# Kernel tuning notes

Measured on AMD Instinct MI355X. Metric: run time of the kernel, lower is better.

Reference implementation:

```python
import jax, jax.numpy as jnp
import numpy as np

B, Z, H, TC, TD, DOUT = 128, 512, 512, 16, 16, 176
DIN_DEC = DOUT + H  # 688: concat(prev_note, conductor_embedding)


def setup_inputs() -> dict:
    key = jax.random.key(0)
    ks = jax.random.split(key, 24)

    def glorot(k, shape):
        lim = np.sqrt(6.0 / (shape[0] + shape[1]))
        return jax.random.uniform(k, shape, jnp.float32, -lim, lim)

    return {
        'z_ssm_embedding': jax.random.normal(ks[0], (B, Z), jnp.float32),
        'pianoroll': jax.random.uniform(ks[1], (B, TC * TD, DOUT), jnp.float32),
        'ssm': jax.random.uniform(ks[2], (B, TC * TD, TC * TD), jnp.float32),
        # z -> conductor initial states (h1,c1,h2,c2), tanh dense
        'Wz': glorot(ks[3], (Z, 4 * H)), 'bz': jnp.zeros((4 * H,), jnp.float32),
        # conductor 2-layer LSTM (input 512)
        'cond_W1': glorot(ks[4], (H, 4 * H)), 'cond_U1': glorot(ks[5], (H, 4 * H)), 'cond_b1': jnp.zeros((4 * H,), jnp.float32),
        'cond_W2': glorot(ks[6], (H, 4 * H)), 'cond_U2': glorot(ks[7], (H, 4 * H)), 'cond_b2': jnp.zeros((4 * H,), jnp.float32),
        # conductor embedding -> decoder initial states, tanh dense
        'Wcd': glorot(ks[8], (H, 4 * H)), 'bcd': jnp.zeros((4 * H,), jnp.float32),
        # core decoder 2-layer LSTM (input 688)
        'dec_W1': glorot(ks[9], (DIN_DEC, 4 * H)), 'dec_U1': glorot(ks[10], (H, 4 * H)), 'dec_b1': jnp.zeros((4 * H,), jnp.float32),
        'dec_W2': glorot(ks[11], (H, 4 * H)), 'dec_U2': glorot(ks[12], (H, 4 * H)), 'dec_b2': jnp.zeros((4 * H,), jnp.float32),
        # output projection (softmax)
        'Wp': glorot(ks[13], (H, DOUT)), 'bp': jnp.zeros((DOUT,), jnp.float32),
    }


def _lstm_step(x, h, c, W, U, b):
    g = x @ W + h @ U + b  # (B, 4H), keras gate order i,f,g,o
    i, f, gg, o = jnp.split(g, 4, axis=-1)
    c = jax.nn.sigmoid(f) * c + jax.nn.sigmoid(i) * jnp.tanh(gg)
    h = jax.nn.sigmoid(o) * jnp.tanh(c)
    return h, c


def reference(z_ssm_embedding, pianoroll, ssm,
              Wz, bz,
              cond_W1, cond_U1, cond_b1, cond_W2, cond_U2, cond_b2,
              Wcd, bcd,
              dec_W1, dec_U1, dec_b1, dec_W2, dec_U2, dec_b2,
              Wp, bp):
    b = z_ssm_embedding.shape[0]
    # conductor initial states from latent (tanh dense, split per layer h/c)
    s = jnp.tanh(z_ssm_embedding @ Wz + bz)
    ch1, cc1, ch2, cc2 = jnp.split(s, 4, axis=-1)
    # In the source, conductor_input and conductor_states are never updated
    # across the outer loop, so the conductor embedding is identical for all
    # 16 segments: compute the single step once.
    x0 = jnp.zeros((b, H), jnp.float32)
    h1, _ = _lstm_step(x0, ch1, cc1, cond_W1, cond_U1, cond_b1)
    cond_emb, _ = _lstm_step(h1, ch2, cc2, cond_W2, cond_U2, cond_b2)  # (B, H)
    # decoder initial states from conductor embedding (same for all segments)
    sd = jnp.tanh(cond_emb @ Wcd + bcd)
    dh1, dc1, dh2, dc2 = jnp.split(sd, 4, axis=-1)

    def seg(note_prev, _):
        def step(carry, _):
            h1, c1, h2, c2, note = carry
            x = jnp.concatenate([note, cond_emb], axis=-1)  # (B, 688)
            h1, c1 = _lstm_step(x, h1, c1, dec_W1, dec_U1, dec_b1)
            h2, c2 = _lstm_step(h1, h2, c2, dec_W2, dec_U2, dec_b2)
            note = jax.nn.softmax(h2 @ Wp + bp, axis=-1)  # output projection
            return (h1, c1, h2, c2, note), note
        (_, _, _, _, note_last), notes = jax.lax.scan(
            step, (dh1, dc1, dh2, dc2, note_prev), None, length=TD)
        return note_last, notes  # notes: (TD, B, DOUT)

    note0 = jnp.zeros((b, DOUT), jnp.float32)
    _, all_notes = jax.lax.scan(seg, note0, None, length=TC)  # (TC, TD, B, DOUT)
    return all_notes.reshape(TC * TD, b, DOUT).transpose(1, 0, 2)  # (B, 256, 176)
```

## Files before the change

### kernel.cpp

```cpp
#include <hip/hip_runtime.h>
#include <hip/hip_bf16.h>
#include <math.h>

#define Bn    128
#define NGn   2048
#define TTn   256
#define DOn   176
#define NBLK  256
#define NTHR  1024
#define HPAR  65536
#define ACC_PAR 24576

typedef unsigned int uint;
using f32x4 = __attribute__((ext_vector_type(4))) float;
using s16x8 = __attribute__((ext_vector_type(8))) short;
union FR { uint u[4]; s16x8 s; };

struct KA {
  const float *z,*Wz,*bz,*cU1,*cb1,*cW2,*cU2,*cb2,*Wcd,*bcd;
  const float *dW1,*dU1,*db1,*dW2,*dU2,*db2,*Wp,*bp;
  float *zT,*sT,*ggate,*h1cT,*ceT,*sdT,*beffP,*db1P,*db2P,*WEp,*out;
  uint *WAh,*WAl,*WBh,*WBl,*h1pk,*h2pk,*dh1pk,*dh2pk;
  int  *accI;
};

__device__ unsigned g_cnt_l1[16 * 32];
__device__ unsigned g_cnt;
__device__ unsigned g_gen;
__device__ unsigned pod_ctr[8 * 64];

__device__ __forceinline__ float sigm(float x) { return 1.0f / (1.0f + __expf(-x)); }

__device__ __forceinline__ float aloadF(const float* p) {
  return __hip_atomic_load(p, __ATOMIC_RELAXED, __HIP_MEMORY_SCOPE_AGENT);
}
__device__ __forceinline__ void astoreF(float* p, float v) {
  __hip_atomic_store(p, v, __ATOMIC_RELAXED, __HIP_MEMORY_SCOPE_AGENT);
}
__device__ __forceinline__ uint aloadU(const uint* p) {
  return __hip_atomic_load(p, __ATOMIC_RELAXED, __HIP_MEMORY_SCOPE_AGENT);
}
__device__ __forceinline__ void astoreU(uint* p, uint v) {
  __hip_atomic_store(p, v, __ATOMIC_RELAXED, __HIP_MEMORY_SCOPE_AGENT);
}
__device__ __forceinline__ int aloadI(const int* p) {
  return __hip_atomic_load(p, __ATOMIC_RELAXED, __HIP_MEMORY_SCOPE_AGENT);
}

__device__ __forceinline__ void split2(float v, unsigned short& h, unsigned short& l) {
  __hip_bfloat16 bh = __float2bfloat16(v);
  float hf = __bfloat162float(bh);
  __hip_bfloat16 bl = __float2bfloat16(v - hf);
  h = *(unsigned short*)&bh; l = *(unsigned short*)&bl;
}
__device__ __forceinline__ uint packsplit(float v) {
  unsigned short h, l; split2(v, h, l);
  return (uint)h | ((uint)l << 16);
}

__device__ __forceinline__ void gbar() {
  __syncthreads();
  if (threadIdx.x == 0) {
    asm volatile("s_waitcnt vmcnt(0)" ::: "memory");
    unsigned g0 = __hip_atomic_load(&g_gen, __ATOMIC_RELAXED, __HIP_MEMORY_SCOPE_AGENT);
    unsigned p1 = __hip_atomic_fetch_add(&g_cnt_l1[(blockIdx.x >> 4) * 32], 1u,
                                         __ATOMIC_RELAXED, __HIP_MEMORY_SCOPE_AGENT);
    if (p1 == 15u) {
      unsigned p2 = __hip_atomic_fetch_add(&g_cnt, 1u, __ATOMIC_RELAXED, __HIP_MEMORY_SCOPE_AGENT);
      if (p2 == 15u) {
        #pragma unroll
        for (int i = 0; i < 16; i++)
          __hip_atomic_store(&g_cnt_l1[i * 32], 0u, __ATOMIC_RELAXED, __HIP_MEMORY_SCOPE_AGENT);
        __hip_atomic_store(&g_cnt, 0u, __ATOMIC_RELAXED, __HIP_MEMORY_SCOPE_AGENT);
        asm volatile("s_waitcnt vmcnt(0)" ::: "memory");
        __hip_atomic_fetch_add(&g_gen, 1u, __ATOMIC_RELAXED, __HIP_MEMORY_SCOPE_AGENT);
      }
    }
    while (__hip_atomic_load(&g_gen, __ATOMIC_RELAXED, __HIP_MEMORY_SCOPE_AGENT) == g0)
      __builtin_amdgcn_s_sleep(1);
  }
  __syncthreads();
}

__device__ __forceinline__ void pbar2(int pod, unsigned& tgt) {
  __syncthreads();
  if (threadIdx.x == 0) {
    asm volatile("s_waitcnt vmcnt(0)" ::: "memory");
    unsigned* ctr = &pod_ctr[pod * 64];
    __hip_atomic_fetch_add(ctr, 1u, __ATOMIC_RELAXED, __HIP_MEMORY_SCOPE_AGENT);
    while ((int)(__hip_atomic_load(ctr, __ATOMIC_RELAXED, __HIP_MEMORY_SCOPE_AGENT) - tgt) < 0) { }
  }
  __syncthreads();
  tgt += 32;
}

__device__ __forceinline__ void stageN(float* __restrict__ xs, const float* __restrict__ X,
                                       int nrows, int b0, int tid) {
  for (int i = tid; i < nrows * 16; i += NTHR)
    xs[i] = aloadF(X + (size_t)(i >> 4) * Bn + b0 + (i & 15));
}

template<int KC>
__device__ __forceinline__ void gemm16(const float* __restrict__ Wb, int colbase,
                                       int kq, int cg, int bg,
                                       const float* __restrict__ xsrc, float acc[16]) {
  const float* wp = Wb + (size_t)(kq * KC) * NGn + colbase + cg * 4;
  const float* xp = xsrc + (kq * KC) * 16 + bg * 4;
  #pragma unroll 2
  for (int kk = 0; kk < KC; kk++) {
    const float4 w4 = *(const float4*)(wp);
    const float4 x4 = *(const float4*)(xp);
    acc[0]  = fmaf(w4.x, x4.x, acc[0]);  acc[1]  = fmaf(w4.x, x4.y, acc[1]);
    acc[2]  = fmaf(w4.x, x4.z, acc[2]);  acc[3]  = fmaf(w4.x, x4.w, acc[3]);
    acc[4]  = fmaf(w4.y, x4.x, acc[4]);  acc[5]  = fmaf(w4.y, x4.y, acc[5]);
    acc[6]  = fmaf(w4.y, x4.z, acc[6]);  acc[7]  = fmaf(w4.y, x4.w, acc[7]);
    acc[8]  = fmaf(w4.z, x4.x, acc[8]);  acc[9]  = fmaf(w4.z, x4.y, acc[9]);
    acc[10] = fmaf(w4.z, x4.z, acc[10]); acc[11] = fmaf(w4.z, x4.w, acc[11]);
    acc[12] = fmaf(w4.w, x4.x, acc[12]); acc[13] = fmaf(w4.w, x4.y, acc[13]);
    acc[14] = fmaf(w4.w, x4.z, acc[14]); acc[15] = fmaf(w4.w, x4.w, acc[15]);
    wp += NGn; xp += 16;
  }
}

__device__ __forceinline__ void pstore(float* __restrict__ part, int kq, int cg, int bg,
                                       const float acc[16]) {
  #pragma unroll
  for (int c = 0; c < 4; c++) {
    float* p = part + (size_t)(kq * 64 + cg * 4 + c) * 17 + bg * 4;
    *(float4*)p = make_float4(acc[c*4], acc[c*4+1], acc[c*4+2], acc[c*4+3]);
  }
}

template<int MODE>
__device__ __forceinline__ void epi_plain(const float* bias, float* out,
                                          int colbase, int b0, int tid,
                                          const float* __restrict__ part) {
  int cl = tid >> 4, bl = tid & 15;
  float s = 0.0f;
  #pragma unroll
  for (int w = 0; w < 8; w++) s += part[(w * 64 + cl) * 17 + bl];
  if (bias) s += bias[colbase + cl];
  if (MODE == 0) s = tanhf(s);
  astoreF(out + (size_t)(colbase + cl) * Bn + b0 + bl, s);
}

__device__ __forceinline__ void cond_nl(const float* gb, const float* cbias,
                                        const float* cin, float* hout, int bid, int tid) {
  int i = bid * NTHR + tid;
  if (i < 512 * Bn) {
    int hid = i >> 7, b = i & 127;
    float gi = aloadF(gb + (size_t)hid * Bn + b)            + cbias[hid];
    float gf = aloadF(gb + (size_t)(512 + hid) * Bn + b)    + cbias[512 + hid];
    float gg = aloadF(gb + (size_t)(1024 + hid) * Bn + b)   + cbias[1024 + hid];
    float go = aloadF(gb + (size_t)(1536 + hid) * Bn + b)   + cbias[1536 + hid];
    float cprev = aloadF(cin + (size_t)hid * Bn + b);
    float c = sigm(gf) * cprev + sigm(gi) * tanhf(gg);
    astoreF(hout + (size_t)hid * Bn + b, sigm(go) * tanhf(c));
  }
}

__device__ __forceinline__ void ldxK(const uint* __restrict__ base, FR& xh, FR& xl) {
  uint w[8];
  #pragma unroll
  for (int e = 0; e < 8; e++) w[e] = aloadU(base + e * 128);
  xh.u[0] = (w[0] & 0xffffu) | (w[1] << 16); xl.u[0] = (w[0] >> 16) | (w[1] & 0xffff0000u);
  xh.u[1] = (w[2] & 0xffffu) | (w[3] << 16); xl.u[1] = (w[2] >> 16) | (w[3] & 0xffff0000u);
  xh.u[2] = (w[4] & 0xffffu) | (w[5] << 16); xl.u[2] = (w[4] >> 16) | (w[5] & 0xffff0000u);
  xh.u[3] = (w[6] & 0xffffu) | (w[7] << 16); xl.u[3] = (w[6] >> 16) | (w[7] & 0xffff0000u);
}
__device__ __forceinline__ void ldxL17(const uint* __restrict__ p, FR& xh, FR& xl) {
  uint w[8];
  #pragma unroll
  for (int e = 0; e < 8; e++) w[e] = p[e * 17];
  xh.u[0] = (w[0] & 0xffffu) | (w[1] << 16); xl.u[0] = (w[0] >> 16) | (w[1] & 0xffff0000u);
  xh.u[1] = (w[2] & 0xffffu) | (w[3] << 16); xl.u[1] = (w[2] >> 16) | (w[3] & 0xffff0000u);
  xh.u[2] = (w[4] & 0xffffu) | (w[5] << 16); xl.u[2] = (w[4] >> 16) | (w[5] & 0xffff0000u);
  xh.u[3] = (w[6] & 0xffffu) | (w[7] << 16); xl.u[3] = (w[6] >> 16) | (w[7] & 0xffff0000u);
}

struct MC {
  const uint *WAh,*WAl,*WBh,*WBl,*dh1pk,*dh2pk;
  uint *h1pk,*h2pk;
  const float *beffP,*db2P,*Wp,*bp;
  int *accI;
  float *out;
  uint *NTu;
  float *plog,*gbuf,*cst,*h2s;
  int j, b0;
};

#define MFMA3(ACC, XH, XL, WH, WL)                                            \
  ACC = __builtin_amdgcn_mfma_f32_16x16x32_bf16(XH.s, WH.s, ACC, 0, 0, 0);    \
  ACC = __builtin_amdgcn_mfma_f32_16x16x32_bf16(XL.s, WH.s, ACC, 0, 0, 0);    \
  ACC = __builtin_amdgcn_mfma_f32_16x16x32_bf16(XH.s, WL.s, ACC, 0, 0, 0);

__device__ __forceinline__ void phaseA(const MC& c, int t, bool doLSTM) {
  const int tid = threadIdx.x, wid = tid >> 6, lane = tid & 63;
  const int m = lane & 15, kh = lane >> 4;
  const int par = t & 1; const bool rst = (t & 15) == 0;
  if (t > 0) {
    const int wv = wid;
    const int* ai = c.accI + ((par ^ 1) * ACC_PAR) + wv * 192;
    float lg[3], pv[3];
    #pragma unroll
    for (int rep = 0; rep < 3; rep++) {
      int o = lane + rep * 64;
      lg[rep] = (o < DOn) ? (float)aloadI(ai + o) * (1.0f / 1048576.0f) + c.bp[o] : -1e30f;
    }
    float mx = fmaxf(fmaxf(lg[0], lg[1]), lg[2]);
    #pragma unroll
    for (int d = 1; d < 64; d <<= 1) mx = fmaxf(mx, __shfl_xor(mx, d));
    float sum = 0.f;
    #pragma unroll
    for (int rep = 0; rep < 3; rep++) {
      int o = lane + rep * 64;
      pv[rep] = (o < DOn) ? __expf(lg[rep] - mx) : 0.f;
      sum += pv[rep];
    }
    #pragma unroll
    for (int d = 1; d < 64; d <<= 1) sum += __shfl_xor(sum, d);
    const float inv = 1.0f / sum;
    #pragma unroll
    for (int rep = 0; rep < 3; rep++) {
      int o = lane + rep * 64;
      float p = pv[rep] * inv;
      c.NTu[o * 17 + wv] = (o < DOn) ? packsplit(p) : 0u;
      if (c.j < 16 && wv == c.j && o < DOn)
        c.out[((size_t)(c.b0 + c.j) * TTn + (t - 1)) * DOn + o] = p;
    }
  }
  __syncthreads();
  if (!doLSTM) return;
  const int nt = wid & 3, ksq = wid >> 2;
  const int s0 = (ksq == 0) ? 0 : (ksq == 1) ? 6 : (ksq == 2) ? 12 : 17;
  const int s1 = (ksq == 0) ? 6 : (ksq == 1) ? 12 : (ksq == 2) ? 17 : 22;
  const uint* hb = (rst ? c.dh1pk : (c.h1pk + (par ^ 1) * HPAR)) + kh * 8 * 128 + c.b0 + m;
  f32x4 acc = {0.f,0.f,0.f,0.f};
  for (int ks = s0; ks < s1; ks++) {
    FR xh, xl;
    if (ks < 6) ldxL17(c.NTu + (ks * 32 + kh * 8) * 17 + m, xh, xl);
    else        ldxK(hb + (ks * 32 - 192) * 128, xh, xl);
    FR wh, wl;
    *(uint4*)wh.u = *(const uint4*)(c.WAh + (size_t)c.j * 22528 + (ks * 4 + nt) * 256 + lane * 4);
    *(uint4*)wl.u = *(const uint4*)(c.WAl + (size_t)c.j * 22528 + (ks * 4 + nt) * 256 + lane * 4);
    MFMA3(acc, xh, xl, wh, wl)
  }
  #pragma unroll
  for (int r = 0; r < 4; r++) c.plog[((ksq * 4 + nt) * 4 + r) * 64 + lane] = acc[r];
  __syncthreads();
  {
    int cl = tid >> 4, bl = tid & 15;
    float s = 0.f;
    #pragma unroll
    for (int k2 = 0; k2 < 4; k2++)
      s += c.plog[((k2 * 4 + (cl >> 4)) * 4 + (bl & 3)) * 64 + (bl >> 2) * 16 + (cl & 15)];
    c.gbuf[cl * 16 + bl] = s + c.beffP[(size_t)(c.j * 64 + cl) * Bn + c.b0 + bl];
  }
  __syncthreads();
  if (tid < 256) {
    int h = tid >> 4, bl = tid & 15;
    float gi = c.gbuf[(h*4+0)*16+bl], gf = c.gbuf[(h*4+1)*16+bl];
    float gg = c.gbuf[(h*4+2)*16+bl], go = c.gbuf[(h*4+3)*16+bl];
    float cp = rst ? c.cst[512 + tid] : c.cst[tid];
    float cc = sigm(gf) * cp + sigm(gi) * tanhf(gg);
    c.cst[tid] = cc;
    astoreU(c.h1pk + par * HPAR + (size_t)(c.j * 16 + h) * 128 + c.b0 + bl,
            packsplit(sigm(go) * tanhf(cc)));
  }
}

__device__ __forceinline__ void phaseB(const MC& c, int t) {
  const int tid = threadIdx.x, wid = tid >> 6, lane = tid & 63;
  const int m = lane & 15, kh = lane >> 4;
  const int nt = wid & 3, ksq = wid >> 2;
  const int par = t & 1; const bool rst = (t & 15) == 0;
  const uint* s1b = c.h1pk + par * HPAR + kh * 8 * 128 + c.b0 + m;
  const uint* s2b = (rst ? c.dh2pk : (c.h2pk + (par ^ 1) * HPAR)) + kh * 8 * 128 + c.b0 + m;
  f32x4 acc = {0.f,0.f,0.f,0.f};
  #pragma unroll
  for (int kk = 0; kk < 8; kk++) {
    const int ks = ksq * 8 + kk;
    FR xh, xl;
    if (ksq < 2) ldxK(s1b + ks * 32 * 128, xh, xl);
    else         ldxK(s2b + (ks - 16) * 32 * 128, xh, xl);
    FR wh, wl;
    *(uint4*)wh.u = *(const uint4*)(c.WBh + (size_t)c.j * 32768 + (ks * 4 + nt) * 256 + lane * 4);
    *(uint4*)wl.u = *(const uint4*)(c.WBl + (size_t)c.j * 32768 + (ks * 4 + nt) * 256 + lane * 4);
    MFMA3(acc, xh, xl, wh, wl)
  }
  #pragma unroll
  for (int r = 0; r < 4; r++) c.plog[((ksq * 4 + nt) * 4 + r) * 64 + lane] = acc[r];
  __syncthreads();
  {
    int cl = tid >> 4, bl = tid & 15;
    float s = 0.f;
    #pragma unroll
    for (int k2 = 0; k2 < 4; k2++)
      s += c.plog[((k2 * 4 + (cl >> 4)) * 4 + (bl & 3)) * 64 + (bl >> 2) * 16 + (cl & 15)];
    c.gbuf[cl * 16 + bl] = s + c.db2P[c.j * 64 + cl];
  }
  __syncthreads();
  if (tid < 256) {
    int h = tid >> 4, bl = tid & 15;
    float gi = c.gbuf[(h*4+0)*16+bl], gf = c.gbuf[(h*4+1)*16+bl];
    float gg = c.gbuf[(h*4+2)*16+bl], go = c.gbuf[(h*4+3)*16+bl];
    float cp = rst ? c.cst[768 + tid] : c.cst[256 + tid];
    float cc = sigm(gf) * cp + sigm(gi) * tanhf(gg);
    c.cst[256 + tid] = cc;
    float h2v = sigm(go) * tanhf(cc);
    c.h2s[h * 16 + bl] = h2v;
    astoreU(c.h2pk + par * HPAR + (size_t)(c.j * 16 + h) * 128 + c.b0 + bl, packsplit(h2v));
  }
  __syncthreads();
  const int o = tid & 255, q = tid >> 8;
  if (o < DOn) {
    float wv[16];
    #pragma unroll
    for (int h = 0; h < 16; h++) wv[h] = c.Wp[(size_t)(c.j * 16 + h) * DOn + o];
    #pragma unroll
    for (int rep = 0; rep < 4; rep++) {
      const int bl = q * 4 + rep;
      float s = 0.f;
      #pragma unroll
      for (int h = 0; h < 16; h++) s = fmaf(c.h2s[h * 16 + bl], wv[h], s);
      __hip_atomic_fetch_add(c.accI + par * ACC_PAR + bl * 192 + o,
                             __float2int_rn(s * 1048576.0f),
                             __ATOMIC_RELAXED, __HIP_MEMORY_SCOPE_AGENT);
    }
  }
  if (tid < 96)
    astoreU((uint*)(c.accI + (par ^ 1) * ACC_PAR + c.j * 96 + tid), 0u);
}

__global__ void __launch_bounds__(NTHR, 1)
hd_kernel(KA A) {
  __shared__ float buf[25088];
  float* xs = buf;
  float* part = buf + 16384;
  const int bid = blockIdx.x, tid = threadIdx.x;
  const int lane = tid & 63;
  const int kqP = tid >> 6, cgP = lane & 15, bgP = lane >> 4;
  const int rP = bid & 31, btP = bid >> 5;
  const int htP = (rP & 7) * 4 + (rP >> 3);
  const int colbaseP = htP * 64, b0P = btP * 16;
  const int pod = bid >> 5;

  unsigned tgt = __hip_atomic_load(&pod_ctr[pod * 64], __ATOMIC_RELAXED,
                                   __HIP_MEMORY_SCOPE_AGENT) + 32;

  {
    const int i0 = bid * NTHR + tid;
    if (i0 < 512 * Bn) { int zb = i0 >> 9, zk = i0 & 511; astoreF(A.zT + (size_t)zk * Bn + zb, A.z[i0]); }
    if (i0 < NGn) {
      int hid = i0 >> 2, g = i0 & 3, sc = g * 512 + hid;
      astoreF(A.db1P + i0, A.db1[sc]);
      astoreF(A.db2P + i0, A.db2[sc]);
    }
    if (i0 < 2 * ACC_PAR) astoreU((uint*)(A.accI + i0), 0u);
    for (int i = i0; i < 512 * NGn; i += NBLK * NTHR) {
      int k = i >> 11, pc = i & 2047;
      int hid = pc >> 2, g = pc & 3;
      astoreF(A.WEp + i, A.dW1[(size_t)(176 + k) * NGn + g * 512 + hid]);
    }
    for (int i = i0; i < 720896; i += NBLK * NTHR) {
      int col = i & 2047, kp = i >> 11, k = kp * 2;
      float w0, w1;
      if (k < 176)      { w0 = A.dW1[(size_t)k * NGn + col];       w1 = A.dW1[(size_t)(k + 1) * NGn + col]; }
      else if (k < 192) { w0 = 0.f; w1 = 0.f; }
      else              { w0 = A.dU1[(size_t)(k - 192) * NGn + col]; w1 = A.dU1[(size_t)(k - 191) * NGn + col]; }
      unsigned short h0, l0, h1, l1; split2(w0, h0, l0); split2(w1, h1, l1);
      int g = col >> 9, hid = col & 511;
      int jj = hid >> 4, cl = (hid & 15) * 4 + g;
      int nt = cl >> 4, n = cl & 15;
      int ks = k >> 5, kr = k & 31, lh = kr >> 3, q = (kr >> 1) & 3;
      int idx = ((jj * 22 + ks) * 4 + nt) * 256 + (lh * 16 + n) * 4 + q;
      astoreU(A.WAh + idx, (uint)h0 | ((uint)h1 << 16));
      astoreU(A.WAl + idx, (uint)l0 | ((uint)l1 << 16));
    }
  }
  gbar();
  {
    stageN(xs, A.zT, 512, b0P, tid); __syncthreads();
    if (tid < 512) {
      float acc[16] = {0,0,0,0,0,0,0,0,0,0,0,0,0,0,0,0};
      gemm16<64>(A.Wz, colbaseP, kqP, cgP, bgP, xs, acc);
      pstore(part, kqP, cgP, bgP, acc);
    }
    __syncthreads();
    epi_plain<0>(A.bz, A.sT, colbaseP, b0P, tid, part);
  }
  gbar();
  {
    stageN(xs, A.sT, 512, b0P, tid); __syncthreads();
    if (tid < 512) {
      float acc[16] = {0,0,0,0,0,0,0,0,0,0,0,0,0,0,0,0};
      gemm16<64>(A.cU1, colbaseP, kqP, cgP, bgP, xs, acc);
      pstore(part, kqP, cgP, bgP, acc);
    }
    __syncthreads();
    epi_plain<1>(nullptr, A.ggate, colbaseP, b0P, tid, part);
  }
  gbar();
  cond_nl(A.ggate, A.cb1, A.sT + (size_t)512 * Bn, A.h1cT, bid, tid);
  gbar();
  {
    stageN(xs, A.h1cT, 512, b0P, tid);
    stageN(xs + 8192, A.sT + (size_t)1024 * Bn, 512, b0P, tid);
    __syncthreads();
    if (tid < 512) {
      float acc[16] = {0,0,0,0,0,0,0,0,0,0,0,0,0,0,0,0};
      gemm16<64>(A.cW2, colbaseP, kqP, cgP, bgP, xs, acc);
      gemm16<64>(A.cU2, colbaseP, kqP, cgP, bgP, xs + 8192, acc);
      pstore(part, kqP, cgP, bgP, acc);
    }
    __syncthreads();
    epi_plain<1>(nullptr, A.ggate, colbaseP, b0P, tid, part);
  }
  gbar();
  cond_nl(A.ggate, A.cb2, A.sT + (size_t)1536 * Bn, A.ceT, bid, tid);
  gbar();
  {
    stageN(xs, A.ceT, 512, b0P, tid); __syncthreads();
    if (tid < 512) {
      float acc[16] = {0,0,0,0,0,0,0,0,0,0,0,0,0,0,0,0};
      gemm16<64>(A.Wcd, colbaseP, kqP, cgP, bgP, xs, acc);
      pstore(part, kqP, cgP, bgP, acc);
    }
    __syncthreads();
    epi_plain<0>(A.bcd, A.sdT, colbaseP, b0P, tid, part);
    __syncthreads();
    if (tid < 512) {
      float acc[16] = {0,0,0,0,0,0,0,0,0,0,0,0,0,0,0,0};
      gemm16<64>(A.WEp, colbaseP, kqP, cgP, bgP, xs, acc);
      pstore(part, kqP, cgP, bgP, acc);
    }
    __syncthreads();
    epi_plain<1>(A.db1P, A.beffP, colbaseP, b0P, tid, part);
  }
  gbar();
  {
    const int i0 = bid * NTHR + tid;
    for (int i = i0; i < 1048576; i += NBLK * NTHR) {
      int col = i & 2047, kp = i >> 11, k = kp * 2;
      float w0, w1;
      if (k < 512) { w0 = A.dW2[(size_t)k * NGn + col];         w1 = A.dW2[(size_t)(k + 1) * NGn + col]; }
      else         { w0 = A.dU2[(size_t)(k - 512) * NGn + col]; w1 = A.dU2[(size_t)(k - 511) * NGn + col]; }
      unsigned short h0, l0, h1, l1; split2(w0, h0, l0); split2(w1, h1, l1);
      int g = col >> 9, hid = col & 511;
      int jj = hid >> 4, cl = (hid & 15) * 4 + g;
      int nt = cl >> 4, n = cl & 15;
      int ks = k >> 5, kr = k & 31, lh = kr >> 3, q = (kr >> 1) & 3;
      int idx = ((jj * 32 + ks) * 4 + nt) * 256 + (lh * 16 + n) * 4 + q;
      astoreU(A.WBh + idx, (uint)h0 | ((uint)h1 << 16));
      astoreU(A.WBl + idx, (uint)l0 | ((uint)l1 << 16));
    }
    if (i0 < 512 * Bn) {
      int hid = i0 >> 7, b = i0 & 127;
      astoreU(A.dh1pk + hid * 128 + b, packsplit(aloadF(A.sdT + (size_t)hid * Bn + b)));
      astoreU(A.dh2pk + hid * 128 + b, packsplit(aloadF(A.sdT + (size_t)(1024 + hid) * Bn + b)));
    }
  }
  gbar();

  MC c;
  c.WAh = A.WAh; c.WAl = A.WAl; c.WBh = A.WBh; c.WBl = A.WBl;
  c.dh1pk = A.dh1pk; c.dh2pk = A.dh2pk;
  c.h1pk = A.h1pk; c.h2pk = A.h2pk;
  c.beffP = A.beffP; c.db2P = A.db2P; c.Wp = A.Wp; c.bp = A.bp; c.out = A.out;
  c.accI = A.accI + pod * 3072;
  c.NTu = (uint*)buf;
  c.plog = buf + 3264;
  c.gbuf = buf + 7360;
  c.cst  = buf + 8384;
  c.h2s  = buf + 9408;
  c.j = bid & 31;
  c.b0 = pod * 16;
  if (tid < 256) {
    int h = tid >> 4, bl = tid & 15;
    c.cst[512 + tid] = aloadF(A.sdT + (size_t)(512 + c.j * 16 + h) * Bn + c.b0 + bl);
    c.cst[768 + tid] = aloadF(A.sdT + (size_t)(1536 + c.j * 16 + h) * Bn + c.b0 + bl);
  }
  for (int i = tid; i < 3264; i += NTHR) c.NTu[i] = 0u;
  __syncthreads();

  for (int t = 0; t < TTn; t++) {
    phaseA(c, t, true);
    pbar2(pod, tgt);
    phaseB(c, t);
    pbar2(pod, tgt);
  }
  phaseA(c, TTn, false);
}

extern "C" void kernel_launch(void* const* d_in, const int* in_sizes, int n_in,
                              void* d_out, int out_size, void* d_ws, size_t ws_size,
                              hipStream_t stream) {
  (void)in_sizes; (void)n_in; (void)out_size; (void)ws_size;
  KA a;
  a.z   = (const float*)d_in[0];
  a.Wz  = (const float*)d_in[3];  a.bz  = (const float*)d_in[4];
  a.cU1 = (const float*)d_in[6];  a.cb1 = (const float*)d_in[7];
  a.cW2 = (const float*)d_in[8];  a.cU2 = (const float*)d_in[9];  a.cb2 = (const float*)d_in[10];
  a.Wcd = (const float*)d_in[11]; a.bcd = (const float*)d_in[12];
  a.dW1 = (const float*)d_in[13]; a.dU1 = (const float*)d_in[14]; a.db1 = (const float*)d_in[15];
  a.dW2 = (const float*)d_in[16]; a.dU2 = (const float*)d_in[17]; a.db2 = (const float*)d_in[18];
  a.Wp  = (const float*)d_in[19]; a.bp  = (const float*)d_in[20];

  float* ws = (float*)d_ws;
  size_t off = 0;
  a.zT    = ws + off; off += (size_t)512  * Bn;
  a.sT    = ws + off; off += (size_t)NGn  * Bn;
  a.ggate = ws + off; off += (size_t)NGn  * Bn;
  a.h1cT  = ws + off; off += (size_t)512  * Bn;
  a.ceT   = ws + off; off += (size_t)512  * Bn;
  a.sdT   = ws + off; off += (size_t)NGn  * Bn;
  a.beffP = ws + off; off += (size_t)NGn  * Bn;
  a.db1P  = ws + off; off += (size_t)NGn;
  a.db2P  = ws + off; off += (size_t)NGn;
  a.WEp   = ws + off; off += (size_t)512 * NGn;
  a.WBh   = (uint*)a.WEp;
  a.WBl   = (uint*)(ws + off); off += (size_t)1048576;
  a.WAh   = (uint*)(ws + off); off += (size_t)720896;
  a.WAl   = (uint*)(ws + off); off += (size_t)720896;
  a.h1pk  = (uint*)(ws + off); off += (size_t)2 * HPAR;
  a.h2pk  = (uint*)(ws + off); off += (size_t)2 * HPAR;
  a.dh1pk = (uint*)(ws + off); off += (size_t)HPAR;
  a.dh2pk = (uint*)(ws + off); off += (size_t)HPAR;
  a.accI  = (int*)(ws + off);  off += (size_t)2 * ACC_PAR;
  a.out   = (float*)d_out;

  hd_kernel<<<dim3(NBLK), dim3(NTHR), 0, stream>>>(a);
}
```

Measured before the change: 7.773 ms.

## Split prep and recurrent decoder into two kernels with 64-block pods

```diff
diff --git a/kernel.cpp b/kernel.cpp
--- a/kernel.cpp
+++ b/kernel.cpp
@@ -7,11 +7,13 @@
 #define TTn   256
 #define DOn   176
 #define NBLK  256
+#define NBLKM 64
 #define NTHR  1024
 #define HPAR  65536
 #define ACC_PAR 24576
 
 typedef unsigned int uint;
+typedef unsigned long long u64;
 using f32x4 = __attribute__((ext_vector_type(4))) float;
 using s16x8 = __attribute__((ext_vector_type(8))) short;
 union FR { uint u[4]; s16x8 s; };
@@ -27,7 +29,7 @@
 __device__ unsigned g_cnt_l1[16 * 32];
 __device__ unsigned g_cnt;
 __device__ unsigned g_gen;
-__device__ unsigned pod_ctr[8 * 64];
+__device__ unsigned pod_slot[8 * 8 * 32];
 
 __device__ __forceinline__ float sigm(float x) { return 1.0f / (1.0f + __expf(-x)); }
 
@@ -44,6 +46,9 @@
   __hip_atomic_store(p, v, __ATOMIC_RELAXED, __HIP_MEMORY_SCOPE_AGENT);
 }
 __device__ __forceinline__ int aloadI(const int* p) {
+  return __hip_atomic_load(p, __ATOMIC_RELAXED, __HIP_MEMORY_SCOPE_AGENT);
+}
+__device__ __forceinline__ u64 aload64(const u64* p) {
   return __hip_atomic_load(p, __ATOMIC_RELAXED, __HIP_MEMORY_SCOPE_AGENT);
 }
 
@@ -82,16 +87,18 @@
   __syncthreads();
 }
 
-__device__ __forceinline__ void pbar2(int pod, unsigned& tgt) {
+__device__ __forceinline__ void pbarS(int pod, int j, unsigned& tgt) {
   __syncthreads();
-  if (threadIdx.x == 0) {
-    asm volatile("s_waitcnt vmcnt(0)" ::: "memory");
-    unsigned* ctr = &pod_ctr[pod * 64];
-    __hip_atomic_fetch_add(ctr, 1u, __ATOMIC_RELAXED, __HIP_MEMORY_SCOPE_AGENT);
-    while ((int)(__hip_atomic_load(ctr, __ATOMIC_RELAXED, __HIP_MEMORY_SCOPE_AGENT) - tgt) < 0) { }
+  if (threadIdx.x < 8) {
+    if (threadIdx.x == 0) {
+      asm volatile("s_waitcnt vmcnt(0)" ::: "memory");
+      astoreU(&pod_slot[(pod * 8 + j) * 32], tgt);
+    }
+    const uint* sl = &pod_slot[(pod * 8 + (int)threadIdx.x) * 32];
+    while ((int)(aloadU(sl) - tgt) < 0) { }
   }
   __syncthreads();
-  tgt += 32;
+  tgt += 1;
 }
 
 __device__ __forceinline__ void stageN(float* __restrict__ xs, const float* __restrict__ X,
@@ -159,181 +166,8 @@
   }
 }
 
-__device__ __forceinline__ void ldxK(const uint* __restrict__ base, FR& xh, FR& xl) {
-  uint w[8];
-  #pragma unroll
-  for (int e = 0; e < 8; e++) w[e] = aloadU(base + e * 128);
-  xh.u[0] = (w[0] & 0xffffu) | (w[1] << 16); xl.u[0] = (w[0] >> 16) | (w[1] & 0xffff0000u);
-  xh.u[1] = (w[2] & 0xffffu) | (w[3] << 16); xl.u[1] = (w[2] >> 16) | (w[3] & 0xffff0000u);
-  xh.u[2] = (w[4] & 0xffffu) | (w[5] << 16); xl.u[2] = (w[4] >> 16) | (w[5] & 0xffff0000u);
-  xh.u[3] = (w[6] & 0xffffu) | (w[7] << 16); xl.u[3] = (w[6] >> 16) | (w[7] & 0xffff0000u);
-}
-__device__ __forceinline__ void ldxL17(const uint* __restrict__ p, FR& xh, FR& xl) {
-  uint w[8];
-  #pragma unroll
-  for (int e = 0; e < 8; e++) w[e] = p[e * 17];
-  xh.u[0] = (w[0] & 0xffffu) | (w[1] << 16); xl.u[0] = (w[0] >> 16) | (w[1] & 0xffff0000u);
-  xh.u[1] = (w[2] & 0xffffu) | (w[3] << 16); xl.u[1] = (w[2] >> 16) | (w[3] & 0xffff0000u);
-  xh.u[2] = (w[4] & 0xffffu) | (w[5] << 16); xl.u[2] = (w[4] >> 16) | (w[5] & 0xffff0000u);
-  xh.u[3] = (w[6] & 0xffffu) | (w[7] << 16); xl.u[3] = (w[6] >> 16) | (w[7] & 0xffff0000u);
-}
-
-struct MC {
-  const uint *WAh,*WAl,*WBh,*WBl,*dh1pk,*dh2pk;
-  uint *h1pk,*h2pk;
-  const float *beffP,*db2P,*Wp,*bp;
-  int *accI;
-  float *out;
-  uint *NTu;
-  float *plog,*gbuf,*cst,*h2s;
-  int j, b0;
-};
-
-#define MFMA3(ACC, XH, XL, WH, WL)                                            \
-  ACC = __builtin_amdgcn_mfma_f32_16x16x32_bf16(XH.s, WH.s, ACC, 0, 0, 0);    \
-  ACC = __builtin_amdgcn_mfma_f32_16x16x32_bf16(XL.s, WH.s, ACC, 0, 0, 0);    \
-  ACC = __builtin_amdgcn_mfma_f32_16x16x32_bf16(XH.s, WL.s, ACC, 0, 0, 0);
-
-__device__ __forceinline__ void phaseA(const MC& c, int t, bool doLSTM) {
-  const int tid = threadIdx.x, wid = tid >> 6, lane = tid & 63;
-  const int m = lane & 15, kh = lane >> 4;
-  const int par = t & 1; const bool rst = (t & 15) == 0;
-  if (t > 0) {
-    const int wv = wid;
-    const int* ai = c.accI + ((par ^ 1) * ACC_PAR) + wv * 192;
-    float lg[3], pv[3];
-    #pragma unroll
-    for (int rep = 0; rep < 3; rep++) {
-      int o = lane + rep * 64;
-      lg[rep] = (o < DOn) ? (float)aloadI(ai + o) * (1.0f / 1048576.0f) + c.bp[o] : -1e30f;
-    }
-    float mx = fmaxf(fmaxf(lg[0], lg[1]), lg[2]);
-    #pragma unroll
-    for (int d = 1; d < 64; d <<= 1) mx = fmaxf(mx, __shfl_xor(mx, d));
-    float sum = 0.f;
-    #pragma unroll
-    for (int rep = 0; rep < 3; rep++) {
-      int o = lane + rep * 64;
-      pv[rep] = (o < DOn) ? __expf(lg[rep] - mx) : 0.f;
-      sum += pv[rep];
-    }
-    #pragma unroll
-    for (int d = 1; d < 64; d <<= 1) sum += __shfl_xor(sum, d);
-    const float inv = 1.0f / sum;
-    #pragma unroll
-    for (int rep = 0; rep < 3; rep++) {
-      int o = lane + rep * 64;
-      float p = pv[rep] * inv;
-      c.NTu[o * 17 + wv] = (o < DOn) ? packsplit(p) : 0u;
-      if (c.j < 16 && wv == c.j && o < DOn)
-        c.out[((size_t)(c.b0 + c.j) * TTn + (t - 1)) * DOn + o] = p;
-    }
-  }
-  __syncthreads();
-  if (!doLSTM) return;
-  const int nt = wid & 3, ksq = wid >> 2;
-  const int s0 = (ksq == 0) ? 0 : (ksq == 1) ? 6 : (ksq == 2) ? 12 : 17;
-  const int s1 = (ksq == 0) ? 6 : (ksq == 1) ? 12 : (ksq == 2) ? 17 : 22;
-  const uint* hb = (rst ? c.dh1pk : (c.h1pk + (par ^ 1) * HPAR)) + kh * 8 * 128 + c.b0 + m;
-  f32x4 acc = {0.f,0.f,0.f,0.f};
-  for (int ks = s0; ks < s1; ks++) {
-    FR xh, xl;
-    if (ks < 6) ldxL17(c.NTu + (ks * 32 + kh * 8) * 17 + m, xh, xl);
-    else        ldxK(hb + (ks * 32 - 192) * 128, xh, xl);
-    FR wh, wl;
-    *(uint4*)wh.u = *(const uint4*)(c.WAh + (size_t)c.j * 22528 + (ks * 4 + nt) * 256 + lane * 4);
-    *(uint4*)wl.u = *(const uint4*)(c.WAl + (size_t)c.j * 22528 + (ks * 4 + nt) * 256 + lane * 4);
-    MFMA3(acc, xh, xl, wh, wl)
-  }
-  #pragma unroll
-  for (int r = 0; r < 4; r++) c.plog[((ksq * 4 + nt) * 4 + r) * 64 + lane] = acc[r];
-  __syncthreads();
-  {
-    int cl = tid >> 4, bl = tid & 15;
-    float s = 0.f;
-    #pragma unroll
-    for (int k2 = 0; k2 < 4; k2++)
-      s += c.plog[((k2 * 4 + (cl >> 4)) * 4 + (bl & 3)) * 64 + (bl >> 2) * 16 + (cl & 15)];
-    c.gbuf[cl * 16 + bl] = s + c.beffP[(size_t)(c.j * 64 + cl) * Bn + c.b0 + bl];
-  }
-  __syncthreads();
-  if (tid < 256) {
-    int h = tid >> 4, bl = tid & 15;
-    float gi = c.gbuf[(h*4+0)*16+bl], gf = c.gbuf[(h*4+1)*16+bl];
-    float gg = c.gbuf[(h*4+2)*16+bl], go = c.gbuf[(h*4+3)*16+bl];
-    float cp = rst ? c.cst[512 + tid] : c.cst[tid];
-    float cc = sigm(gf) * cp + sigm(gi) * tanhf(gg);
-    c.cst[tid] = cc;
-    astoreU(c.h1pk + par * HPAR + (size_t)(c.j * 16 + h) * 128 + c.b0 + bl,
-            packsplit(sigm(go) * tanhf(cc)));
-  }
-}
-
-__device__ __forceinline__ void phaseB(const MC& c, int t) {
-  const int tid = threadIdx.x, wid = tid >> 6, lane = tid & 63;
-  const int m = lane & 15, kh = lane >> 4;
-  const int nt = wid & 3, ksq = wid >> 2;
-  const int par = t & 1; const bool rst = (t & 15) == 0;
-  const uint* s1b = c.h1pk + par * HPAR + kh * 8 * 128 + c.b0 + m;
-  const uint* s2b = (rst ? c.dh2pk : (c.h2pk + (par ^ 1) * HPAR)) + kh * 8 * 128 + c.b0 + m;
-  f32x4 acc = {0.f,0.f,0.f,0.f};
-  #pragma unroll
-  for (int kk = 0; kk < 8; kk++) {
-    const int ks = ksq * 8 + kk;
-    FR xh, xl;
-    if (ksq < 2) ldxK(s1b + ks * 32 * 128, xh, xl);
-    else         ldxK(s2b + (ks - 16) * 32 * 128, xh, xl);
-    FR wh, wl;
-    *(uint4*)wh.u = *(const uint4*)(c.WBh + (size_t)c.j * 32768 + (ks * 4 + nt) * 256 + lane * 4);
-    *(uint4*)wl.u = *(const uint4*)(c.WBl + (size_t)c.j * 32768 + (ks * 4 + nt) * 256 + lane * 4);
-    MFMA3(acc, xh, xl, wh, wl)
-  }
-  #pragma unroll
-  for (int r = 0; r < 4; r++) c.plog[((ksq * 4 + nt) * 4 + r) * 64 + lane] = acc[r];
-  __syncthreads();
-  {
-    int cl = tid >> 4, bl = tid & 15;
-    float s = 0.f;
-    #pragma unroll
-    for (int k2 = 0; k2 < 4; k2++)
-      s += c.plog[((k2 * 4 + (cl >> 4)) * 4 + (bl & 3)) * 64 + (bl >> 2) * 16 + (cl & 15)];
-    c.gbuf[cl * 16 + bl] = s + c.db2P[c.j * 64 + cl];
-  }
-  __syncthreads();
-  if (tid < 256) {
-    int h = tid >> 4, bl = tid & 15;
-    float gi = c.gbuf[(h*4+0)*16+bl], gf = c.gbuf[(h*4+1)*16+bl];
-    float gg = c.gbuf[(h*4+2)*16+bl], go = c.gbuf[(h*4+3)*16+bl];
-    float cp = rst ? c.cst[768 + tid] : c.cst[256 + tid];
-    float cc = sigm(gf) * cp + sigm(gi) * tanhf(gg);
-    c.cst[256 + tid] = cc;
-    float h2v = sigm(go) * tanhf(cc);
-    c.h2s[h * 16 + bl] = h2v;
-    astoreU(c.h2pk + par * HPAR + (size_t)(c.j * 16 + h) * 128 + c.b0 + bl, packsplit(h2v));
-  }
-  __syncthreads();
-  const int o = tid & 255, q = tid >> 8;
-  if (o < DOn) {
-    float wv[16];
-    #pragma unroll
-    for (int h = 0; h < 16; h++) wv[h] = c.Wp[(size_t)(c.j * 16 + h) * DOn + o];
-    #pragma unroll
-    for (int rep = 0; rep < 4; rep++) {
-      const int bl = q * 4 + rep;
-      float s = 0.f;
-      #pragma unroll
-      for (int h = 0; h < 16; h++) s = fmaf(c.h2s[h * 16 + bl], wv[h], s);
-      __hip_atomic_fetch_add(c.accI + par * ACC_PAR + bl * 192 + o,
-                             __float2int_rn(s * 1048576.0f),
-                             __ATOMIC_RELAXED, __HIP_MEMORY_SCOPE_AGENT);
-    }
-  }
-  if (tid < 96)
-    astoreU((uint*)(c.accI + (par ^ 1) * ACC_PAR + c.j * 96 + tid), 0u);
-}
-
 __global__ void __launch_bounds__(NTHR, 1)
-hd_kernel(KA A) {
+hd_prep(KA A) {
   __shared__ float buf[25088];
   float* xs = buf;
   float* part = buf + 16384;
@@ -343,10 +177,6 @@
   const int rP = bid & 31, btP = bid >> 5;
   const int htP = (rP & 7) * 4 + (rP >> 3);
   const int colbaseP = htP * 64, b0P = btP * 16;
-  const int pod = bid >> 5;
-
-  unsigned tgt = __hip_atomic_load(&pod_ctr[pod * 64], __ATOMIC_RELAXED,
-                                   __HIP_MEMORY_SCOPE_AGENT) + 32;
 
   {
     const int i0 = bid * NTHR + tid;
@@ -370,10 +200,11 @@
       else              { w0 = A.dU1[(size_t)(k - 192) * NGn + col]; w1 = A.dU1[(size_t)(k - 191) * NGn + col]; }
       unsigned short h0, l0, h1, l1; split2(w0, h0, l0); split2(w1, h1, l1);
       int g = col >> 9, hid = col & 511;
-      int jj = hid >> 4, cl = (hid & 15) * 4 + g;
-      int nt = cl >> 4, n = cl & 15;
+      int jb = hid >> 6;
+      int jcol = (hid & 63) * 4 + g;
+      int nt = jcol >> 4, n = jcol & 15;
       int ks = k >> 5, kr = k & 31, lh = kr >> 3, q = (kr >> 1) & 3;
-      int idx = ((jj * 22 + ks) * 4 + nt) * 256 + (lh * 16 + n) * 4 + q;
+      int idx = ((jb * 22 + ks) * 16 + nt) * 256 + (lh * 16 + n) * 4 + q;
       astoreU(A.WAh + idx, (uint)h0 | ((uint)h1 << 16));
       astoreU(A.WAl + idx, (uint)l0 | ((uint)l1 << 16));
     }
@@ -447,49 +278,233 @@
       else         { w0 = A.dU2[(size_t)(k - 512) * NGn + col]; w1 = A.dU2[(size_t)(k - 511) * NGn + col]; }
       unsigned short h0, l0, h1, l1; split2(w0, h0, l0); split2(w1, h1, l1);
       int g = col >> 9, hid = col & 511;
-      int jj = hid >> 4, cl = (hid & 15) * 4 + g;
-      int nt = cl >> 4, n = cl & 15;
+      int jb = hid >> 6;
+      int jcol = (hid & 63) * 4 + g;
+      int nt = jcol >> 4, n = jcol & 15;
       int ks = k >> 5, kr = k & 31, lh = kr >> 3, q = (kr >> 1) & 3;
-      int idx = ((jj * 32 + ks) * 4 + nt) * 256 + (lh * 16 + n) * 4 + q;
+      int idx = ((jb * 32 + ks) * 16 + nt) * 256 + (lh * 16 + n) * 4 + q;
       astoreU(A.WBh + idx, (uint)h0 | ((uint)h1 << 16));
       astoreU(A.WBl + idx, (uint)l0 | ((uint)l1 << 16));
     }
     if (i0 < 512 * Bn) {
       int hid = i0 >> 7, b = i0 & 127;
-      astoreU(A.dh1pk + hid * 128 + b, packsplit(aloadF(A.sdT + (size_t)hid * Bn + b)));
-      astoreU(A.dh2pk + hid * 128 + b, packsplit(aloadF(A.sdT + (size_t)(1024 + hid) * Bn + b)));
-    }
-  }
-  gbar();
-
-  MC c;
-  c.WAh = A.WAh; c.WAl = A.WAl; c.WBh = A.WBh; c.WBl = A.WBl;
-  c.dh1pk = A.dh1pk; c.dh2pk = A.dh2pk;
-  c.h1pk = A.h1pk; c.h2pk = A.h2pk;
-  c.beffP = A.beffP; c.db2P = A.db2P; c.Wp = A.Wp; c.bp = A.bp; c.out = A.out;
-  c.accI = A.accI + pod * 3072;
-  c.NTu = (uint*)buf;
-  c.plog = buf + 3264;
-  c.gbuf = buf + 7360;
-  c.cst  = buf + 8384;
-  c.h2s  = buf + 9408;
-  c.j = bid & 31;
-  c.b0 = pod * 16;
-  if (tid < 256) {
-    int h = tid >> 4, bl = tid & 15;
-    c.cst[512 + tid] = aloadF(A.sdT + (size_t)(512 + c.j * 16 + h) * Bn + c.b0 + bl);
-    c.cst[768 + tid] = aloadF(A.sdT + (size_t)(1536 + c.j * 16 + h) * Bn + c.b0 + bl);
-  }
-  for (int i = tid; i < 3264; i += NTHR) c.NTu[i] = 0u;
+      astoreU(A.dh1pk + ((size_t)((hid >> 3) * 128 + b)) * 8 + (hid & 7),
+              packsplit(aloadF(A.sdT + (size_t)hid * Bn + b)));
+      astoreU(A.dh2pk + ((size_t)((hid >> 3) * 128 + b)) * 8 + (hid & 7),
+              packsplit(aloadF(A.sdT + (size_t)(1024 + hid) * Bn + b)));
+    }
+  }
+}
+
+__device__ __forceinline__ void unpackL17(const uint* __restrict__ p, FR& xh, FR& xl) {
+  uint w[8];
+  #pragma unroll
+  for (int e = 0; e < 8; e++) w[e] = p[e * 17];
+  xh.u[0] = (w[0] & 0xffffu) | (w[1] << 16); xl.u[0] = (w[0] >> 16) | (w[1] & 0xffff0000u);
+  xh.u[1] = (w[2] & 0xffffu) | (w[3] << 16); xl.u[1] = (w[2] >> 16) | (w[3] & 0xffff0000u);
+  xh.u[2] = (w[4] & 0xffffu) | (w[5] << 16); xl.u[2] = (w[4] >> 16) | (w[5] & 0xffff0000u);
+  xh.u[3] = (w[6] & 0xffffu) | (w[7] << 16); xl.u[3] = (w[6] >> 16) | (w[7] & 0xffff0000u);
+}
+
+#define MFMA3(ACC, XH, XL, WH, WL)                                            \
+  ACC = __builtin_amdgcn_mfma_f32_16x16x32_bf16(XH.s, WH.s, ACC, 0, 0, 0);    \
+  ACC = __builtin_amdgcn_mfma_f32_16x16x32_bf16(XL.s, WH.s, ACC, 0, 0, 0);    \
+  ACC = __builtin_amdgcn_mfma_f32_16x16x32_bf16(XH.s, WL.s, ACC, 0, 0, 0);
+
+__device__ __forceinline__ void stage512(uint* __restrict__ SB, int r0,
+                                         const uint* __restrict__ src, int b0, int tid) {
+  const int kt = tid >> 4, bl = tid & 15;
+  const u64* p = (const u64*)src + ((size_t)(kt * 128 + b0 + bl)) * 4;
+  u64 d0 = aload64(p), d1 = aload64(p + 1), d2 = aload64(p + 2), d3 = aload64(p + 3);
+  uint* q = SB + (r0 + kt * 8) * 17 + bl;
+  q[0 * 17] = (uint)d0; q[1 * 17] = (uint)(d0 >> 32);
+  q[2 * 17] = (uint)d1; q[3 * 17] = (uint)(d1 >> 32);
+  q[4 * 17] = (uint)d2; q[5 * 17] = (uint)(d2 >> 32);
+  q[6 * 17] = (uint)d3; q[7 * 17] = (uint)(d3 >> 32);
+}
+
+__global__ void __launch_bounds__(NTHR, 1)
+hd_main(KA A) {
+  __shared__ float buf[32512];
+  uint*  SB  = (uint*)buf;
+  uint*  NT  = (uint*)(buf + 17408);
+  float* gb  = buf + 20672;
+  float* cst = buf + 25024;
+  float* h2s = buf + 27072;
+  float* beffL = buf + 28160;
+  float* db2L  = buf + 32256;
+
+  const int bid = blockIdx.x, tid = threadIdx.x;
+  const int wid = tid >> 6, lane = tid & 63;
+  const int m = lane & 15, kh = lane >> 4;
+  const int j = bid & 7, pod = bid >> 3;
+  const int b0 = pod * 16;
+  const int nt = wid;
+
+  unsigned tgt = aloadU(&pod_slot[(pod * 8 + j) * 32]) + 1;
+
+  #pragma unroll
+  for (int r = 0; r < 4; r++) {
+    int idx = tid + r * NTHR;
+    int cl = idx >> 4, bl = idx & 15;
+    beffL[idx] = aloadF(A.beffP + (size_t)(j * 256 + cl) * Bn + b0 + bl);
+  }
+  if (tid < 256) db2L[tid] = A.db2P[j * 256 + tid];
+  #pragma unroll
+  for (int r = 0; r < 4; r++) {
+    int idx = tid + r * NTHR;
+    if (idx < 3264) NT[idx] = 0u;
+  }
   __syncthreads();
 
-  for (int t = 0; t < TTn; t++) {
-    phaseA(c, t, true);
-    pbar2(pod, tgt);
-    phaseB(c, t);
-    pbar2(pod, tgt);
-  }
-  phaseA(c, TTn, false);
+  int* accI = A.accI + pod * 3072;
+
+  for (int t = 0; t <= TTn; t++) {
+    const int par = t & 1;
+    const bool rst = (t & 15) == 0;
+    const bool last = (t == TTn);
+
+    if (t > 0) {
+      const int* ai = accI + ((par ^ 1) * ACC_PAR) + wid * 192 + lane;
+      int a0 = aloadI(ai), a1 = aloadI(ai + 64), a2 = aloadI(ai + 128);
+      float lg[3], pv[3];
+      lg[0] = (lane < DOn)       ? (float)a0 * (1.0f/1048576.0f) + A.bp[lane]       : -1e30f;
+      lg[1] = (lane+64 < DOn)    ? (float)a1 * (1.0f/1048576.0f) + A.bp[lane+64]    : -1e30f;
+      lg[2] = (lane+128 < DOn)   ? (float)a2 * (1.0f/1048576.0f) + A.bp[lane+128]   : -1e30f;
+      float mx = fmaxf(fmaxf(lg[0], lg[1]), lg[2]);
+      #pragma unroll
+      for (int d = 1; d < 64; d <<= 1) mx = fmaxf(mx, __shfl_xor(mx, d));
+      float sum = 0.f;
+      #pragma unroll
+      for (int rep = 0; rep < 3; rep++) {
+        int o = lane + rep * 64;
+        pv[rep] = (o < DOn) ? __expf(lg[rep] - mx) : 0.f;
+        sum += pv[rep];
+      }
+      #pragma unroll
+      for (int d = 1; d < 64; d <<= 1) sum += __shfl_xor(sum, d);
+      const float inv = 1.0f / sum;
+      #pragma unroll
+      for (int rep = 0; rep < 3; rep++) {
+        int o = lane + rep * 64;
+        if (o < 192) {
+          float p = pv[rep] * inv;
+          NT[o * 17 + wid] = (o < DOn) ? packsplit(p) : 0u;
+          if ((wid & 7) == j && o < DOn)
+            A.out[((size_t)(b0 + wid) * TTn + (t - 1)) * DOn + o] = p;
+        }
+      }
+    }
+    if (last) break;
+
+    stage512(SB, 512, rst ? A.dh2pk : (A.h2pk + (par ^ 1) * HPAR), b0, tid);
+    if (rst) stage512(SB, 0, A.dh1pk, b0, tid);
+    __syncthreads();
+
+    {
+      const uint* WH = A.WAh + (size_t)j * 90112;
+      const uint* WL = A.WAl + (size_t)j * 90112;
+      f32x4 a0 = {0,0,0,0}, a1 = {0,0,0,0};
+      for (int ks = 0; ks < 22; ks += 2) {
+        FR xh, xl, wh, wl;
+        const uint* xp0 = (ks < 6) ? (NT + (ks * 32 + kh * 8) * 17 + m)
+                                   : (SB + ((ks - 6) * 32 + kh * 8) * 17 + m);
+        unpackL17(xp0, xh, xl);
+        *(uint4*)wh.u = *(const uint4*)(WH + (ks * 16 + nt) * 256 + lane * 4);
+        *(uint4*)wl.u = *(const uint4*)(WL + (ks * 16 + nt) * 256 + lane * 4);
+        MFMA3(a0, xh, xl, wh, wl)
+        const int k2 = ks + 1;
+        const uint* xp1 = (k2 < 6) ? (NT + (k2 * 32 + kh * 8) * 17 + m)
+                                   : (SB + ((k2 - 6) * 32 + kh * 8) * 17 + m);
+        unpackL17(xp1, xh, xl);
+        *(uint4*)wh.u = *(const uint4*)(WH + (k2 * 16 + nt) * 256 + lane * 4);
+        *(uint4*)wl.u = *(const uint4*)(WL + (k2 * 16 + nt) * 256 + lane * 4);
+        MFMA3(a1, xh, xl, wh, wl)
+      }
+      #pragma unroll
+      for (int r = 0; r < 4; r++)
+        gb[(nt * 16 + (lane & 15)) * 17 + kh * 4 + r] = a0[r] + a1[r];
+    }
+    __syncthreads();
+    {
+      const int hl = tid >> 4, bl = tid & 15;
+      float g4[4];
+      #pragma unroll
+      for (int g = 0; g < 4; g++)
+        g4[g] = gb[(hl * 4 + g) * 17 + bl] + beffL[(hl * 4 + g) * 16 + bl];
+      const int hid = j * 64 + hl;
+      float cp = rst ? aloadF(A.sdT + (size_t)(512 + hid) * Bn + b0 + bl) : cst[tid];
+      float cc = sigm(g4[1]) * cp + sigm(g4[0]) * tanhf(g4[2]);
+      cst[tid] = cc;
+      astoreU(A.h1pk + par * HPAR + ((size_t)((hid >> 3) * 128 + b0 + bl)) * 8 + (hid & 7),
+              packsplit(sigm(g4[3]) * tanhf(cc)));
+    }
+    pbarS(pod, j, tgt);
+
+    stage512(SB, 0, A.h1pk + par * HPAR, b0, tid);
+    __syncthreads();
+
+    {
+      const uint* WH = A.WBh + (size_t)j * 131072;
+      const uint* WL = A.WBl + (size_t)j * 131072;
+      f32x4 a0 = {0,0,0,0}, a1 = {0,0,0,0};
+      for (int ks = 0; ks < 32; ks += 2) {
+        FR xh, xl, wh, wl;
+        unpackL17(SB + (ks * 32 + kh * 8) * 17 + m, xh, xl);
+        *(uint4*)wh.u = *(const uint4*)(WH + (ks * 16 + nt) * 256 + lane * 4);
+        *(uint4*)wl.u = *(const uint4*)(WL + (ks * 16 + nt) * 256 + lane * 4);
+        MFMA3(a0, xh, xl, wh, wl)
+        unpackL17(SB + ((ks + 1) * 32 + kh * 8) * 17 + m, xh, xl);
+        *(uint4*)wh.u = *(const uint4*)(WH + ((ks + 1) * 16 + nt) * 256 + lane * 4);
+        *(uint4*)wl.u = *(const uint4*)(WL + ((ks + 1) * 16 + nt) * 256 + lane * 4);
+        MFMA3(a1, xh, xl, wh, wl)
+      }
+      #pragma unroll
+      for (int r = 0; r < 4; r++)
+        gb[(nt * 16 + (lane & 15)) * 17 + kh * 4 + r] = a0[r] + a1[r];
+    }
+    __syncthreads();
+    {
+      const int hl = tid >> 4, bl = tid & 15;
+      float g4[4];
+      #pragma unroll
+      for (int g = 0; g < 4; g++)
+        g4[g] = gb[(hl * 4 + g) * 17 + bl] + db2L[hl * 4 + g];
+      const int hid = j * 64 + hl;
+      float cp = rst ? aloadF(A.sdT + (size_t)(1536 + hid) * Bn + b0 + bl) : cst[1024 + tid];
+      float cc = sigm(g4[1]) * cp + sigm(g4[0]) * tanhf(g4[2]);
+      cst[1024 + tid] = cc;
+      float h2v = sigm(g4[3]) * tanhf(cc);
+      h2s[hl * 17 + bl] = h2v;
+      astoreU(A.h2pk + par * HPAR + ((size_t)((hid >> 3) * 128 + b0 + bl)) * 8 + (hid & 7),
+              packsplit(h2v));
+    }
+    __syncthreads();
+    {
+      const int o = tid & 255, q = tid >> 8;
+      if (o < DOn) {
+        float s0 = 0.f, s1 = 0.f, s2 = 0.f, s3 = 0.f;
+        for (int h = 0; h < 64; h++) {
+          const float w = A.Wp[(size_t)(j * 64 + h) * DOn + o];
+          s0 = fmaf(h2s[h * 17 + q * 4 + 0], w, s0);
+          s1 = fmaf(h2s[h * 17 + q * 4 + 1], w, s1);
+          s2 = fmaf(h2s[h * 17 + q * 4 + 2], w, s2);
+          s3 = fmaf(h2s[h * 17 + q * 4 + 3], w, s3);
+        }
+        __hip_atomic_fetch_add(accI + par * ACC_PAR + (q * 4 + 0) * 192 + o,
+                               __float2int_rn(s0 * 1048576.0f), __ATOMIC_RELAXED, __HIP_MEMORY_SCOPE_AGENT);
+        __hip_atomic_fetch_add(accI + par * ACC_PAR + (q * 4 + 1) * 192 + o,
+                               __float2int_rn(s1 * 1048576.0f), __ATOMIC_RELAXED, __HIP_MEMORY_SCOPE_AGENT);
+        __hip_atomic_fetch_add(accI + par * ACC_PAR + (q * 4 + 2) * 192 + o,
+                               __float2int_rn(s2 * 1048576.0f), __ATOMIC_RELAXED, __HIP_MEMORY_SCOPE_AGENT);
+        __hip_atomic_fetch_add(accI + par * ACC_PAR + (q * 4 + 3) * 192 + o,
+                               __float2int_rn(s3 * 1048576.0f), __ATOMIC_RELAXED, __HIP_MEMORY_SCOPE_AGENT);
+      }
+      if (tid < 384)
+        astoreU((uint*)(accI + (par ^ 1) * ACC_PAR + j * 384 + tid), 0u);
+    }
+    pbarS(pod, j, tgt);
+  }
 }
 
 extern "C" void kernel_launch(void* const* d_in, const int* in_sizes, int n_in,
@@ -529,5 +544,6 @@
   a.accI  = (int*)(ws + off);  off += (size_t)2 * ACC_PAR;
   a.out   = (float*)d_out;
 
-  hd_kernel<<<dim3(NBLK), dim3(NTHR), 0, stream>>>(a);
-}
+  hd_prep<<<dim3(NBLK),  dim3(NTHR), 0, stream>>>(a);
+  hd_main<<<dim3(NBLKM), dim3(NTHR), 0, stream>>>(a);
+}
```

Result: slower. 17.60 ms (+126.4%).
